# Performance work log

Measured on AMD Instinct MI355X. Metric: run time of the kernel, lower is better.

Reference implementation:

```python
import jax, jax.numpy as jnp
import numpy as np
from jax import lax

KH, KW, K = 3, 3, 9
PAD, BN_EPS = 1, 1e-5


def setup_inputs() -> dict:
    key = jax.random.key(0)
    ks = jax.random.split(key, 10)
    B, CHI, CHO, H, W = 2, 64, 64, 128, 128
    x = jax.random.normal(ks[0], (B, CHI, H, W), dtype=jnp.float32)
    # offset/mask branch conv: 3*K output channels (o1, o2, mask)
    w_off = jax.random.normal(ks[1], (3 * K, CHI, KH, KW), dtype=jnp.float32) * 0.01
    b_off = jax.random.normal(ks[2], (3 * K,), dtype=jnp.float32) * 0.01
    # main deformable conv weight/bias
    fan = CHI * K
    weight = jax.random.normal(ks[3], (CHO, CHI, KH, KW), dtype=jnp.float32) / np.sqrt(fan)
    bias = jax.random.normal(ks[4], (CHO,), dtype=jnp.float32) * 0.01
    # BatchNorm (eval-mode) params
    gamma = jax.random.uniform(ks[5], (CHO,), minval=0.5, maxval=1.5, dtype=jnp.float32)
    beta = jax.random.normal(ks[6], (CHO,), dtype=jnp.float32) * 0.1
    run_mean = jax.random.normal(ks[7], (CHO,), dtype=jnp.float32) * 0.1
    run_var = jax.random.uniform(ks[8], (CHO,), minval=0.5, maxval=1.5, dtype=jnp.float32)
    return {"x": x, "w_off": w_off, "b_off": b_off, "weight": weight,
            "bias": bias, "gamma": gamma, "beta": beta,
            "run_mean": run_mean, "run_var": run_var}


def _dcn_bn_relu(x, w_off, b_off, weight, bias, gamma, beta, run_mean, run_var):
    B, C, H, W = x.shape
    CHO = weight.shape[0]
    # offset/mask branch: regular 3x3 conv, stride 1, pad 1
    om = lax.conv_general_dilated(
        x, w_off, window_strides=(1, 1), padding=[(PAD, PAD), (PAD, PAD)],
        dimension_numbers=("NCHW", "OIHW", "NCHW")) + b_off[None, :, None, None]
    o1, o2, m = jnp.split(om, 3, axis=1)          # each [B, K, H, W]
    offset = jnp.concatenate([o1, o2], axis=1)    # [B, 2K, H, W]
    off_y = offset[:, 0::2]                       # interleaved (y, x) per tap, as in DCNv2 CUDA
    off_x = offset[:, 1::2]
    mask = jax.nn.sigmoid(m)                      # [B, K, H, W] modulation

    # sampling positions: p = p0 + p_k + offset
    ky, kx = jnp.meshgrid(jnp.arange(KH), jnp.arange(KW), indexing="ij")
    ky = ky.reshape(K).astype(x.dtype)
    kx = kx.reshape(K).astype(x.dtype)
    hh = jnp.arange(H, dtype=x.dtype)
    ww = jnp.arange(W, dtype=x.dtype)
    py = hh[None, None, :, None] - PAD + ky[None, :, None, None] + off_y  # [B,K,H,W]
    px = ww[None, None, None, :] - PAD + kx[None, :, None, None] + off_x

    y0f = jnp.floor(py)
    x0f = jnp.floor(px)
    ly = (py - y0f)[..., None]
    lx = (px - x0f)[..., None]
    y0 = y0f.astype(jnp.int32)
    x0 = x0f.astype(jnp.int32)
    bidx = jnp.arange(B)[:, None, None, None]

    def gather(yi, xi):
        valid = ((yi >= 0) & (yi < H) & (xi >= 0) & (xi < W)).astype(x.dtype)
        yc = jnp.clip(yi, 0, H - 1)
        xc = jnp.clip(xi, 0, W - 1)
        g = x[bidx, :, yc, xc]                    # [B, K, H, W, C]
        return g * valid[..., None]

    v00 = gather(y0, x0)
    v01 = gather(y0, x0 + 1)
    v10 = gather(y0 + 1, x0)
    v11 = gather(y0 + 1, x0 + 1)
    sampled = (v00 * (1 - ly) * (1 - lx) + v01 * (1 - ly) * lx
               + v10 * ly * (1 - lx) + v11 * ly * lx)
    sampled = sampled * mask[..., None]           # modulated

    out = jnp.einsum("bkhwc,ock->bohw", sampled,
                     weight.reshape(CHO, C, K)) + bias[None, :, None, None]

    # eval-mode BatchNorm + ReLU
    inv = gamma / jnp.sqrt(run_var + BN_EPS)
    out = (out - run_mean[None, :, None, None]) * inv[None, :, None, None] \
          + beta[None, :, None, None]
    return jax.nn.relu(out)


def reference(x, w_off, b_off, weight, bias, gamma, beta, run_mean, run_var):
    return _dcn_bn_relu(x, w_off, b_off, weight, bias, gamma, beta, run_mean, run_var)
```

## Files before the change

kernel.cpp:

```cpp
#include <hip/hip_runtime.h>
#include <hip/hip_bf16.h>

#define HH 128
#define WW 128
#define CI 64
#define CO 64
#define SLS 584
#define HPS 72
#define HALW 18

typedef __attribute__((ext_vector_type(8))) short short8;
typedef __attribute__((ext_vector_type(4))) float floatx4;

__device__ __forceinline__ unsigned short f2bf(float f) {
  union { float f; unsigned u; } uu; uu.f = f;
  unsigned r = uu.u + 0x7FFFu + ((uu.u >> 16) & 1u);
  return (unsigned short)(r >> 16);
}
__device__ __forceinline__ unsigned pack2bf(float lo, float hi) {
  return (unsigned)f2bf(lo) | ((unsigned)f2bf(hi) << 16);
}
__device__ __forceinline__ float bfl(unsigned u) { return __uint_as_float(u << 16); }
__device__ __forceinline__ float bfh(unsigned u) { return __uint_as_float(u & 0xffff0000u); }

__global__ __launch_bounds__(256) void prep_kernel(
    const float* __restrict__ x, unsigned* __restrict__ xTb_u,
    const float* __restrict__ weight, const float* __restrict__ bias,
    const float* __restrict__ gamma, const float* __restrict__ beta,
    const float* __restrict__ mean, const float* __restrict__ var,
    const float* __restrict__ w_off, const float* __restrict__ b_off,
    unsigned short* __restrict__ Wm, unsigned short* __restrict__ w2,
    float* __restrict__ bias2, float* __restrict__ boff2) {
  __shared__ unsigned T2[32 * 33];
  int bid = blockIdx.x;
  int tid = threadIdx.x;
  if (bid < 1024) {
    int b = bid >> 9, h = (bid >> 2) & 127, q = bid & 3;
    int cp = tid >> 3, wc = tid & 7;
    const float* xp = x + (((long)(b * CI + 2 * cp) * HH + h) * WW + q * 32 + wc * 4);
    float4 a0 = *(const float4*)xp;
    float4 a1 = *(const float4*)(xp + HH * WW);
    T2[(wc * 4 + 0) * 33 + cp] = pack2bf(a0.x, a1.x);
    T2[(wc * 4 + 1) * 33 + cp] = pack2bf(a0.y, a1.y);
    T2[(wc * 4 + 2) * 33 + cp] = pack2bf(a0.z, a1.z);
    T2[(wc * 4 + 3) * 33 + cp] = pack2bf(a0.w, a1.w);
    __syncthreads();
    int px = tid >> 3, g = tid & 7;
    const unsigned* src = &T2[px * 33 + g * 4];
    unsigned* dst = xTb_u + ((long)((b * HH + h) * WW + q * 32 + px)) * 32 + g * 4;
    *(uint4*)dst = make_uint4(src[0], src[1], src[2], src[3]);
    return;
  }
  int idx = (bid - 1024) * 256 + tid;
  if (idx < 32) boff2[idx] = (idx < 27) ? b_off[idx] : 0.f;
  if (idx >= CO * 576) return;
  int o = idx / 576, kc = idx - o * 576;
  int k = kc >> 6, c = kc & 63;
  float inv = gamma[o] * rsqrtf(var[o] + 1e-5f);
  Wm[idx] = f2bf(weight[(o * CI + c) * 9 + k] * inv);
  if (kc == 0) bias2[o] = (bias[o] - mean[o]) * inv + beta[o];
  if (o < 27) w2[idx] = f2bf(w_off[o * 576 + c * 9 + k]);
  else if (o < 32) w2[idx] = 0;
}

__global__ __launch_bounds__(256, 4) void dcn_kernel(
    const unsigned short* __restrict__ xTb,
    const unsigned short* __restrict__ w2, const float* __restrict__ boff2,
    const unsigned short* __restrict__ Wm, const float* __restrict__ bias2,
    float* __restrict__ out) {
  __shared__ char smem[26752];
  short* hal = (short*)smem;
  __hip_bfloat16* SL = (__hip_bfloat16*)smem;
  float* omL = (float*)(smem + 18688);
  float4* Pw = (float4*)(smem + 23296);
  int2* Po = (int2*)(smem + 25600);

  int bid = blockIdx.x;
  int s = bid & 7;
  int n = bid >> 3;
  int b = n >> 7;
  int rem = n & 127;
  int h = s * 16 + (rem >> 3);
  int w0 = (rem & 7) * 16;
  int tid = threadIdx.x, lane = tid & 63, wave = tid >> 6;

#pragma unroll
  for (int it = 0; it < 2; it++) {
    int t = it * 256 + tid;
    if (t < 432) {
      int row = t / 144;
      int r2 = t - row * 144;
      int xi = r2 >> 3, cg = r2 & 7;
      int y = h - 1 + row, xx = w0 - 1 + xi;
      uint4 v = make_uint4(0u, 0u, 0u, 0u);
      if ((unsigned)y < (unsigned)HH && (unsigned)xx < (unsigned)WW)
        v = *(const uint4*)(xTb + (long)((b * HH + y) * WW + xx) * CI + cg * 8);
      *(uint4*)(hal + (row * HALW + xi) * HPS + cg * 8) = v;
    }
  }
  __syncthreads();

  {
    int r16 = lane & 15, quad = lane >> 4;
    int m16 = wave & 1, kh = wave >> 1;
    floatx4 t0 = {0.f, 0.f, 0.f, 0.f};
    floatx4 t1 = {0.f, 0.f, 0.f, 0.f};
    if (kh == 0) t0 = *(const floatx4*)(boff2 + m16 * 16 + quad * 4);
    const short* ap = (const short*)(w2 + (m16 * 16 + r16) * 576 + kh * 32 + quad * 8);
#pragma unroll
    for (int kk = 0; kk < 9; kk++) {
      int dy = kk / 3, dxk = kk - 3 * (kk / 3);
      short8 bfrag = *(const short8*)(hal + (dy * HALW + r16 + dxk) * HPS + kh * 32 + quad * 8);
      short8 afrag = *(const short8*)(ap + kk * 64);
      if (kk & 1)
        t1 = __builtin_amdgcn_mfma_f32_16x16x32_bf16(afrag, bfrag, t1, 0, 0, 0);
      else
        t0 = __builtin_amdgcn_mfma_f32_16x16x32_bf16(afrag, bfrag, t0, 0, 0, 0);
    }
    floatx4 t = t0 + t1;
    *(floatx4*)(omL + kh * 576 + r16 * 36 + m16 * 16 + quad * 4) = t;
  }
  __syncthreads();

  if (lane < 36) {
    int p_loc = (lane * 7282) >> 16;
    int k = lane - p_loc * 9;
    int p = wave * 4 + p_loc;
    const float* o0 = omL + p * 36;
    const float* o1 = omL + 576 + p * 36;
    float oy = o0[2 * k] + o1[2 * k];
    float ox = o0[2 * k + 1] + o1[2 * k + 1];
    float mm = o0[18 + k] + o1[18 + k];
    float msk = 1.f / (1.f + __expf(-mm));
    int ky = (k * 11) >> 5;
    int kx = k - 3 * ky;
    float py = (float)(h - 1 + ky) + oy;
    float pxx = (float)(w0 + p - 1 + kx) + ox;
    float y0f = floorf(py), x0f = floorf(pxx);
    float ly = py - y0f, lx = pxx - x0f;
    int y0 = (int)y0f, x0 = (int)x0f;
    int y1 = y0 + 1, x1 = x0 + 1;
    float lylx = ly * lx;
    bool y0v = (unsigned)y0 < (unsigned)HH, y1v = (unsigned)y1 < (unsigned)HH;
    bool x0v = (unsigned)x0 < (unsigned)WW, x1v = (unsigned)x1 < (unsigned)WW;
    int yc0 = min(max(y0, 0), HH - 1), yc1 = min(max(y1, 0), HH - 1);
    int xc0 = min(max(x0, 0), WW - 1), xc1 = min(max(x1, 0), WW - 1);
    Pw[p * 9 + k] = make_float4((y0v && x0v) ? (1.f - ly - lx + lylx) * msk : 0.f,
                                (y0v && x1v) ? (lx - lylx) * msk : 0.f,
                                (y1v && x0v) ? (ly - lylx) * msk : 0.f,
                                (y1v && x1v) ? lylx * msk : 0.f);
    int dxs = (xc1 - xc0) * CI;
    int dys = (yc1 - yc0) * WW * CI;
    Po[p * 9 + k] = make_int2((yc0 * WW + xc0) * CI, dxs | (dys << 16));
  }

  {
    int cq = lane & 15, pl = lane >> 4;
    int p = wave * 4 + pl;
    const unsigned short* xb = xTb + (long)b * (HH * WW * CI);
    uint2 u[9][4];
#pragma unroll
    for (int k = 0; k < 9; k++) {
      int2 po = Po[p * 9 + k];
      int o00 = po.x + cq * 4;
      int dx = po.y & 0xffff;
      int dyv = po.y >> 16;
      u[k][0] = *(const uint2*)(xb + o00);
      u[k][1] = *(const uint2*)(xb + o00 + dx);
      u[k][2] = *(const uint2*)(xb + o00 + dyv);
      u[k][3] = *(const uint2*)(xb + o00 + dyv + dx);
    }
#pragma unroll
    for (int k = 0; k < 9; k++) {
      float4 wv = Pw[p * 9 + k];
      uint2 u00 = u[k][0], u01 = u[k][1], u10 = u[k][2], u11 = u[k][3];
      float lo0 = bfl(u00.x) * wv.x + bfl(u01.x) * wv.y + bfl(u10.x) * wv.z + bfl(u11.x) * wv.w;
      float hi0 = bfh(u00.x) * wv.x + bfh(u01.x) * wv.y + bfh(u10.x) * wv.z + bfh(u11.x) * wv.w;
      float lo1 = bfl(u00.y) * wv.x + bfl(u01.y) * wv.y + bfl(u10.y) * wv.z + bfl(u11.y) * wv.w;
      float hi1 = bfh(u00.y) * wv.x + bfh(u01.y) * wv.y + bfh(u10.y) * wv.z + bfh(u11.y) * wv.w;
      *(uint2*)(&SL[p * SLS + k * 64 + cq * 4]) =
          make_uint2(pack2bf(lo0, hi0), pack2bf(lo1, hi1));
    }
  }
  __syncthreads();

  {
    int r16 = lane & 15, quad = lane >> 4;
    floatx4 acc0 = *(const floatx4*)(bias2 + wave * 16 + quad * 4);
    floatx4 acc1 = {0.f, 0.f, 0.f, 0.f};
    const unsigned short* Ap = Wm + (wave * 16 + r16) * 576 + quad * 8;
    const __hip_bfloat16* Sp = &SL[r16 * SLS + quad * 8];
#pragma unroll
    for (int kc0 = 0; kc0 < 576; kc0 += 64) {
      short8 av0 = *(const short8*)(Ap + kc0);
      short8 bv0 = *(const short8*)(Sp + kc0);
      acc0 = __builtin_amdgcn_mfma_f32_16x16x32_bf16(av0, bv0, acc0, 0, 0, 0);
      short8 av1 = *(const short8*)(Ap + kc0 + 32);
      short8 bv1 = *(const short8*)(Sp + kc0 + 32);
      acc1 = __builtin_amdgcn_mfma_f32_16x16x32_bf16(av1, bv1, acc1, 0, 0, 0);
    }
    floatx4 acc = acc0 + acc1;
#pragma unroll
    for (int r = 0; r < 4; r++) {
      int o = wave * 16 + quad * 4 + r;
      out[((b * CO + o) * HH + h) * WW + w0 + r16] = fmaxf(acc[r], 0.f);
    }
  }
}

extern "C" void kernel_launch(void* const* d_in, const int* in_sizes, int n_in,
                              void* d_out, int out_size, void* d_ws, size_t ws_size,
                              hipStream_t stream) {
  const float* x = (const float*)d_in[0];
  const float* w_off = (const float*)d_in[1];
  const float* b_off = (const float*)d_in[2];
  const float* weight = (const float*)d_in[3];
  const float* bias = (const float*)d_in[4];
  const float* gamma = (const float*)d_in[5];
  const float* beta = (const float*)d_in[6];
  const float* run_mean = (const float*)d_in[7];
  const float* run_var = (const float*)d_in[8];
  float* outp = (float*)d_out;

  char* ws = (char*)d_ws;
  unsigned* xTb = (unsigned*)ws;
  unsigned short* Wm = (unsigned short*)(ws + 4194304);
  unsigned short* w2 = (unsigned short*)(ws + 4268032);
  float* bias2 = (float*)(ws + 4304896);
  float* boff2 = (float*)(ws + 4305152);

  prep_kernel<<<1168, 256, 0, stream>>>(x, xTb, weight, bias, gamma, beta,
                                        run_mean, run_var, w_off, b_off,
                                        Wm, w2, bias2, boff2);
  dcn_kernel<<<2048, 256, 0, stream>>>((const unsigned short*)xTb, w2, boff2,
                                       Wm, bias2, outp);
}
```

Before: 112.5 us.

## Pass per-tap sampling weights and offsets via wave shuffles, shrink LDS, raise occupancy

The per-tap bilinear weights and gather offsets are now kept in registers and broadcast to consumer lanes with __shfl, instead of being staged through LDS. Each offset is packed into a single int (20-bit base plus one bit each for the dx and dy steps). With the Pw/Po buffers gone and omL overlapped onto the SL region, shared memory per block drops from 26752 to 18688 bytes. The launch-bounds occupancy hint rises from 4 to 8 blocks. The aim is to cut LDS traffic and fit more blocks per CU, at the cost of an extra barrier and tighter VGPR budgets that could cause spills given the 72-register gather buffer.

```diff
diff --git a/kernel.cpp b/kernel.cpp
--- a/kernel.cpp
+++ b/kernel.cpp
@@ -63,17 +63,15 @@
   else if (o < 32) w2[idx] = 0;
 }
 
-__global__ __launch_bounds__(256, 4) void dcn_kernel(
+__global__ __launch_bounds__(256, 8) void dcn_kernel(
     const unsigned short* __restrict__ xTb,
     const unsigned short* __restrict__ w2, const float* __restrict__ boff2,
     const unsigned short* __restrict__ Wm, const float* __restrict__ bias2,
     float* __restrict__ out) {
-  __shared__ char smem[26752];
+  __shared__ char smem[18688];
   short* hal = (short*)smem;
   __hip_bfloat16* SL = (__hip_bfloat16*)smem;
-  float* omL = (float*)(smem + 18688);
-  float4* Pw = (float4*)(smem + 23296);
-  int2* Po = (int2*)(smem + 25600);
+  float* omL = (float*)(smem + 14016);
 
   int bid = blockIdx.x;
   int s = bid & 7;
@@ -109,7 +107,7 @@
     const short* ap = (const short*)(w2 + (m16 * 16 + r16) * 576 + kh * 32 + quad * 8);
 #pragma unroll
     for (int kk = 0; kk < 9; kk++) {
-      int dy = kk / 3, dxk = kk - 3 * (kk / 3);
+      int dy = kk / 3, dxk = kk - 3 * dy;
       short8 bfrag = *(const short8*)(hal + (dy * HALW + r16 + dxk) * HPS + kh * 32 + quad * 8);
       short8 afrag = *(const short8*)(ap + kk * 64);
       if (kk & 1)
@@ -122,6 +120,8 @@
   }
   __syncthreads();
 
+  float pwx = 0.f, pwy = 0.f, pwz = 0.f, pww = 0.f;
+  int pov = 0;
   if (lane < 36) {
     int p_loc = (lane * 7282) >> 16;
     int k = lane - p_loc * 9;
@@ -145,14 +145,16 @@
     bool x0v = (unsigned)x0 < (unsigned)WW, x1v = (unsigned)x1 < (unsigned)WW;
     int yc0 = min(max(y0, 0), HH - 1), yc1 = min(max(y1, 0), HH - 1);
     int xc0 = min(max(x0, 0), WW - 1), xc1 = min(max(x1, 0), WW - 1);
-    Pw[p * 9 + k] = make_float4((y0v && x0v) ? (1.f - ly - lx + lylx) * msk : 0.f,
-                                (y0v && x1v) ? (lx - lylx) * msk : 0.f,
-                                (y1v && x0v) ? (ly - lylx) * msk : 0.f,
-                                (y1v && x1v) ? lylx * msk : 0.f);
+    pwx = (y0v && x0v) ? (1.f - ly - lx + lylx) * msk : 0.f;
+    pwy = (y0v && x1v) ? (lx - lylx) * msk : 0.f;
+    pwz = (y1v && x0v) ? (ly - lylx) * msk : 0.f;
+    pww = (y1v && x1v) ? lylx * msk : 0.f;
+    int off00 = (yc0 * WW + xc0) * CI;
     int dxs = (xc1 - xc0) * CI;
     int dys = (yc1 - yc0) * WW * CI;
-    Po[p * 9 + k] = make_int2((yc0 * WW + xc0) * CI, dxs | (dys << 16));
-  }
+    pov = off00 | ((dxs >> 6) << 20) | ((dys >> 13) << 21);
+  }
+  __syncthreads();
 
   {
     int cq = lane & 15, pl = lane >> 4;
@@ -161,10 +163,10 @@
     uint2 u[9][4];
 #pragma unroll
     for (int k = 0; k < 9; k++) {
-      int2 po = Po[p * 9 + k];
-      int o00 = po.x + cq * 4;
-      int dx = po.y & 0xffff;
-      int dyv = po.y >> 16;
+      int v = __shfl(pov, pl * 9 + k);
+      int o00 = (v & 0xFFFFF) + cq * 4;
+      int dx = (v >> 14) & 64;
+      int dyv = (v >> 8) & 8192;
       u[k][0] = *(const uint2*)(xb + o00);
       u[k][1] = *(const uint2*)(xb + o00 + dx);
       u[k][2] = *(const uint2*)(xb + o00 + dyv);
@@ -172,12 +174,16 @@
     }
 #pragma unroll
     for (int k = 0; k < 9; k++) {
-      float4 wv = Pw[p * 9 + k];
+      int src = pl * 9 + k;
+      float wx = __shfl(pwx, src);
+      float wy = __shfl(pwy, src);
+      float wz = __shfl(pwz, src);
+      float ww = __shfl(pww, src);
       uint2 u00 = u[k][0], u01 = u[k][1], u10 = u[k][2], u11 = u[k][3];
-      float lo0 = bfl(u00.x) * wv.x + bfl(u01.x) * wv.y + bfl(u10.x) * wv.z + bfl(u11.x) * wv.w;
-      float hi0 = bfh(u00.x) * wv.x + bfh(u01.x) * wv.y + bfh(u10.x) * wv.z + bfh(u11.x) * wv.w;
-      float lo1 = bfl(u00.y) * wv.x + bfl(u01.y) * wv.y + bfl(u10.y) * wv.z + bfl(u11.y) * wv.w;
-      float hi1 = bfh(u00.y) * wv.x + bfh(u01.y) * wv.y + bfh(u10.y) * wv.z + bfh(u11.y) * wv.w;
+      float lo0 = bfl(u00.x) * wx + bfl(u01.x) * wy + bfl(u10.x) * wz + bfl(u11.x) * ww;
+      float hi0 = bfh(u00.x) * wx + bfh(u01.x) * wy + bfh(u10.x) * wz + bfh(u11.x) * ww;
+      float lo1 = bfl(u00.y) * wx + bfl(u01.y) * wy + bfl(u10.y) * wz + bfl(u11.y) * ww;
+      float hi1 = bfh(u00.y) * wx + bfh(u01.y) * wy + bfh(u10.y) * wz + bfh(u11.y) * ww;
       *(uint2*)(&SL[p * SLS + k * 64 + cq * 4]) =
           make_uint2(pack2bf(lo0, hi0), pack2bf(lo1, hi1));
     }
```

After: 112.7 us. About the same (+0.2%).
